# Optimization experiments

Hardware: AMD Instinct MI355X
Metric: run time of the kernel (lower is better)

The kernel has to match this reference:

```python
import jax, jax.numpy as jnp
import numpy as np

V = 6          # num_variables
K = 6          # codebook_size
D = 32         # embedding_dim
C = 3          # channels
B = 64         # batch
N = K ** V     # 46656 codebook combinations
EPS = 1e-5     # torch BatchNorm eps
ENTROPY_SCALE = 0.1


def setup_inputs() -> dict:
    key = jax.random.key(0)
    ks = jax.random.split(key, 40)
    i = iter(range(40))
    def rn(shape, s):
        return jax.random.normal(ks[next(i)], shape, dtype=jnp.float32) * s
    def rv(shape):
        return 0.5 + 0.5 * jax.random.uniform(ks[next(i)], shape, dtype=jnp.float32)
    inp = {
        'x': jax.random.normal(ks[next(i)], (B, C, 7, 7), dtype=jnp.float32),
        # encoder
        'conv_w': rn((256, C, 7, 7), 0.08), 'conv_b': rn((256,), 0.01),
        'ebn2_g': 1.0 + rn((256,), 0.1), 'ebn2_b': rn((256,), 0.1),
        'fc1_w': rn((1024, 256), 0.06), 'fc1_b': rn((1024,), 0.01),
        'ebn1_g': 1.0 + rn((1024,), 0.1), 'ebn1_b': rn((1024,), 0.1),
        'fc2_w': rn((V * K, 1024), 0.03), 'fc2_b': rn((V * K,), 0.01),
        # quantizer embeddings (V separate codebooks)
        'embeds': jax.random.normal(ks[next(i)], (V, K, D), dtype=jnp.float32),
        # decoder
        'dfc1_w': rn((1024, V * D), 0.07), 'dfc1_b': rn((1024,), 0.01),
        'dbn1_g': 1.0 + rn((1024,), 0.1), 'dbn1_b': rn((1024,), 0.1),
        'dbn1_rm': rn((1024,), 0.1), 'dbn1_rv': rv((1024,)),
        'dfc2_w': rn((256, 1024), 0.03), 'dfc2_b': rn((256,), 0.01),
        'dbn2_g': 1.0 + rn((256,), 0.1), 'dbn2_b': rn((256,), 0.1),
        'dbn2_rm': rn((256,), 0.1), 'dbn2_rv': rv((256,)),
        'dct1_w': rn((256, 16, 7, 7), 0.05), 'dct1_b': rn((16,), 0.01),
        'dbn3_g': 1.0 + rn((16,), 0.1), 'dbn3_b': rn((16,), 0.1),
        'dbn3_rm': rn((16,), 0.1), 'dbn3_rv': rv((16,)),
        'dct2_w': rn((16, C), 0.2), 'dct2_b': rn((C,), 0.01),
    }
    return inp


def _bn_eval(t, g, b, rm, rvar):
    # eval-mode BatchNorm (running stats); params broadcast over leading dims
    return g * (t - rm) * jax.lax.rsqrt(rvar + EPS) + b


def _bn_train(t, g, b):
    # train-mode BatchNorm1d on (B, F): biased batch statistics over dim 0
    m = t.mean(0)
    v = ((t - m) ** 2).mean(0)
    return g * (t - m) * jax.lax.rsqrt(v + EPS) + b


def _decode_all(embeds, dfc1_w, dfc1_b, dbn1_g, dbn1_b, dbn1_rm, dbn1_rv,
                dfc2_w, dfc2_b, dbn2_g, dbn2_b, dbn2_rm, dbn2_rv,
                dct1_w, dct1_b, dbn3_g, dbn3_b, dbn3_rm, dbn3_rv,
                dct2_w, dct2_b):
    # enumerate all K^V index tuples in itertools.product order (first var slowest)
    idx = jnp.arange(N)
    powers = K ** (V - 1 - jnp.arange(V))
    combos = (idx[:, None] // powers[None, :]) % K          # (N, V)
    z = embeds[jnp.arange(V)[None, :], combos]              # (N, V, D) gather
    h = z.reshape(N, V * D) @ dfc1_w.T + dfc1_b             # (N, 1024)
    h = jax.nn.relu(_bn_eval(h, dbn1_g, dbn1_b, dbn1_rm, dbn1_rv))
    h = h @ dfc2_w.T + dfc2_b                               # (N, 256)
    h = jax.nn.relu(_bn_eval(h, dbn2_g, dbn2_b, dbn2_rm, dbn2_rv))
    # ConvTranspose2d(256,16,7,stride=2) on 1x1 input == einsum with full kernel
    h = jnp.einsum('ni,iohw->nohw', h, dct1_w) + dct1_b[:, None, None]  # (N,16,7,7)
    h = jax.nn.relu(_bn_eval(h, dbn3_g[:, None, None], dbn3_b[:, None, None],
                             dbn3_rm[:, None, None], dbn3_rv[:, None, None]))
    # ConvTranspose2d(16,C,1,1) == pointwise channel mix
    em = jnp.einsum('nihw,io->nohw', h, dct2_w) + dct2_b[:, None, None]  # (N,C,7,7)
    return em


def reference(x, conv_w, conv_b, ebn2_g, ebn2_b, fc1_w, fc1_b, ebn1_g, ebn1_b,
              fc2_w, fc2_b, embeds, dfc1_w, dfc1_b, dbn1_g, dbn1_b, dbn1_rm,
              dbn1_rv, dfc2_w, dfc2_b, dbn2_g, dbn2_b, dbn2_rm, dbn2_rv,
              dct1_w, dct1_b, dbn3_g, dbn3_b, dbn3_rm, dbn3_rv, dct2_w, dct2_b):
    # emission means for every codebook combination (batched decode, BN eval)
    em = _decode_all(embeds, dfc1_w, dfc1_b, dbn1_g, dbn1_b, dbn1_rm, dbn1_rv,
                     dfc2_w, dfc2_b, dbn2_g, dbn2_b, dbn2_rm, dbn2_rv,
                     dct1_w, dct1_b, dbn3_g, dbn3_b, dbn3_rm, dbn3_rv,
                     dct2_w, dct2_b)                         # (N, C, 7, 7)
    # encoder: Conv2d(C,256,7) on 7x7 input collapses to a single GEMM
    e = jnp.einsum('bchw,ochw->bo', x, conv_w) + conv_b      # (B, 256)
    e = jax.nn.relu(_bn_train(e, ebn2_g, ebn2_b))
    e = e @ fc1_w.T + fc1_b                                  # (B, 1024)
    e = jax.nn.relu(_bn_train(e, ebn1_g, ebn1_b))
    logits = e @ fc2_w.T + fc2_b                             # (B, V*K)
    # quantizer
    latent_dist = jax.nn.softmax(logits.reshape(B, V, K), axis=-1)
    latent_loss = ENTROPY_SCALE * jnp.sum(
        latent_dist * jnp.log(latent_dist + 1e-10), axis=(1, 2))
    # obs logits: -0.5 * ||em - x||^2 summed over (C,H,W), via expanded form
    E = em.reshape(N, -1)                                    # (N, 147)
    X = x.reshape(B, -1)                                     # (B, 147)
    obs = -0.5 * (jnp.sum(E * E, -1)[None, :]
                  - 2.0 * (X @ E.T)
                  + jnp.sum(X * X, -1)[:, None])             # (B, N)
    obs_logits = obs.reshape((B,) + (K,) * V)
    return obs_logits, latent_dist, latent_loss
```

## Files before the change

kernel.cpp:

```cpp
#include <hip/hip_runtime.h>
#include <math.h>

#define EPSF 1e-5f
#define NNC 46656

typedef __attribute__((ext_vector_type(4))) float  f32x4;
typedef __attribute__((ext_vector_type(8))) short  short8;
typedef __attribute__((ext_vector_type(8))) unsigned short ushort8;
typedef __attribute__((ext_vector_type(4))) unsigned int uint4v;

__device__ __forceinline__ float bf2f(unsigned short u) {
    unsigned int x = ((unsigned int)u) << 16;
    return __builtin_bit_cast(float, x);
}
__device__ __forceinline__ unsigned short f2bf(float f) {
    unsigned int x = __builtin_bit_cast(unsigned int, f);
    unsigned int r = (x + 0x7fffu + ((x >> 16) & 1u)) >> 16;
    return (unsigned short)r;
}

__device__ __forceinline__ short8 packrelu8(ushort8 H8, ushort8 S8) {
    uint4v H = __builtin_bit_cast(uint4v, H8);
    uint4v S = __builtin_bit_cast(uint4v, S8);
    uint4v O;
#pragma unroll
    for (int d = 0; d < 4; ++d) {
        float hlo = __builtin_bit_cast(float, H[d] << 16);
        float hhi = __builtin_bit_cast(float, H[d] & 0xffff0000u);
        float slo = __builtin_bit_cast(float, S[d] << 16);
        float shi = __builtin_bit_cast(float, S[d] & 0xffff0000u);
        unsigned int rlo = __builtin_bit_cast(unsigned int, fmaxf(hlo + slo, 0.f));
        unsigned int rhi = __builtin_bit_cast(unsigned int, fmaxf(hhi + shi, 0.f));
        O[d] = __builtin_amdgcn_perm(rhi, rlo, 0x07060302u);
    }
    return __builtin_bit_cast(short8, O);
}

#define WS_SH    37888u
#define WS_S3    148480u
#define WS_W2BF  259072u
#define WS_C2    390144u
#define WS_W3BF  390400u
#define WS_C3    490752u
#define WS_XBF   490768u
#define WS_SX2   495888u
#define WS_E1T   495952u
#define WS_E2T   512336u
#define WS_FLAG  577872u

#define OBS_SIZE (64*NNC)
#define DIST_OFF OBS_SIZE
#define LOSS_OFF (OBS_SIZE + 64*36)

#define LDS_BYTES 75008


__global__ void dvae_k1(const float* __restrict__ x,
                        const float* __restrict__ conv_w, const float* __restrict__ conv_b,
                        const float* __restrict__ ebn2_g, const float* __restrict__ ebn2_b,
                        const float* __restrict__ embeds, const float* __restrict__ dfc1_w,
                        const float* __restrict__ dfc1_b,
                        const float* __restrict__ dbn1_g, const float* __restrict__ dbn1_b,
                        const float* __restrict__ dbn1_rm, const float* __restrict__ dbn1_rv,
                        const float* __restrict__ dfc2_w, const float* __restrict__ dfc2_b,
                        const float* __restrict__ dbn2_g, const float* __restrict__ dbn2_b,
                        const float* __restrict__ dbn2_rm, const float* __restrict__ dbn2_rv,
                        const float* __restrict__ dct1_w, const float* __restrict__ dct1_b,
                        const float* __restrict__ dbn3_g, const float* __restrict__ dbn3_b,
                        const float* __restrict__ dbn3_rm, const float* __restrict__ dbn3_rv,
                        float* __restrict__ ws) {
    __shared__ float sbuf[12544];
    int bx = blockIdx.x, tid = threadIdx.x;
    if (bx < 64) {
        float* wtile = sbuf;
        float* semb  = sbuf + 3088;
        float* Pt    = sbuf + 4240;
        float* c1s   = sbuf + 4960;
        int j0 = bx * 16;
        for (int e = tid; e < 16 * 192; e += 256)
            wtile[(e / 192) * 193 + (e % 192)] = dfc1_w[j0 * 192 + e];
        for (int e = tid; e < 1152; e += 256) semb[e] = embeds[e];
        __syncthreads();
        for (int e = tid; e < 576; e += 256) {
            int vk = e >> 4, jL = e & 15;
            int v = vk / 6;
            int j = j0 + jL;
            const float* wrow = &wtile[jL * 193 + v * 32];
            const float* ep = &semb[vk * 32];
            float dot = 0.f;
#pragma unroll
            for (int d = 0; d < 32; ++d) dot += wrow[d] * ep[d];
            float s1 = dbn1_g[j] * rsqrtf(dbn1_rv[j] + EPSF);
            Pt[vk * 20 + jL] = s1 * dot;
        }
        if (tid < 16) {
            int j = j0 + tid;
            float s = dbn1_g[j] * rsqrtf(dbn1_rv[j] + EPSF);
            c1s[tid] = s * dfc1_b[j] + dbn1_b[j] - dbn1_rm[j] * s;
        }
        __syncthreads();
        unsigned short* Sh = (unsigned short*)(ws + WS_SH);
        unsigned short* S3 = (unsigned short*)(ws + WS_S3);
        for (int e = tid; e < 216 * 16; e += 256) {
            int gh = e >> 4, jL = e & 15;
            int d0 = gh / 36, d1 = (gh / 6) % 6, d2 = gh % 6;
            float vh = c1s[jL] + Pt[d0 * 20 + jL] + Pt[(6 + d1) * 20 + jL] + Pt[(12 + d2) * 20 + jL];
            float vs = Pt[(18 + d0) * 20 + jL] + Pt[(24 + d1) * 20 + jL] + Pt[(30 + d2) * 20 + jL];
            Sh[gh * 1024 + j0 + jL] = f2bf(vh);
            S3[gh * 1024 + j0 + jL] = f2bf(vs);
        }
    } else if (bx < 320) {
        int t = (bx - 64) * 256 + tid;
        int i = t >> 8, kq = (t & 255) * 4;
        float s2 = dbn2_g[i] * rsqrtf(dbn2_rv[i] + EPSF);
        float4 w = *(const float4*)(dfc2_w + i * 1024 + kq);
        unsigned short* dst = (unsigned short*)(ws + WS_W2BF) + i * 1024 + kq;
        dst[0] = f2bf(s2 * w.x); dst[1] = f2bf(s2 * w.y);
        dst[2] = f2bf(s2 * w.z); dst[3] = f2bf(s2 * w.w);
        if (kq == 0) ws[WS_C2 + i] = s2 * dfc2_b[i] + dbn2_b[i] - dbn2_rm[i] * s2;
    } else if (bx < 336) {
        int blk = bx - 320;
        for (int e = tid; e < 12544; e += 256) sbuf[e] = dct1_w[blk * 12544 + e];
        __syncthreads();
        unsigned short* W3 = (unsigned short*)(ws + WS_W3BF);
        for (int e = tid; e < 1568; e += 256) {
            int up = e >> 1, k8 = (e & 1) * 8;
            int o = up & 15, hw = up >> 4;
            float s3 = dbn3_g[o] * rsqrtf(dbn3_rv[o] + EPSF);
            ushort8 ov;
#pragma unroll
            for (int t2 = 0; t2 < 8; ++t2)
                ov[t2] = f2bf(s3 * sbuf[(k8 + t2) * 784 + o * 49 + hw]);
            *(ushort8*)(W3 + up * 256 + blk * 16 + k8) = ov;
        }
        if (blk == 0 && tid < 16) {
            float s = dbn3_g[tid] * rsqrtf(dbn3_rv[tid] + EPSF);
            ws[WS_C3 + tid] = s * dct1_b[tid] + dbn3_b[tid] - dbn3_rm[tid] * s;
        }
    } else if (bx == 336) {
        unsigned short* Xb = (unsigned short*)(ws + WS_XBF);
        if (tid == 0) *(int*)(ws + WS_FLAG) = 0;
        if (tid < 64) {
            const float* xp = x + tid * 147;
            float s = 0.f;
            for (int qq = 0; qq < 147; ++qq) { float v = xp[qq]; s += v * v; }
            ws[WS_SX2 + tid] = s;
        }
        for (int e = tid; e < 64 * 160; e += 256) {
            int b = e / 160, col = e % 160;
            float v = 0.f;
            if (col < 147) { int hw = col / 3, c = col % 3; v = x[b * 147 + c * 49 + hw]; }
            Xb[e] = f2bf(v);
        }
    } else {
        int blk = bx - 337;
        for (int e = tid; e < 9408; e += 256) sbuf[e] = x[e];
        __syncthreads();
        int b = tid & 63;
        int oL = __builtin_amdgcn_readfirstlane(tid >> 6);
        int o = blk * 4 + oL;
        const float* wp = conv_w + o * 147;
        float acc = conv_b[o];
#pragma unroll 7
        for (int qq = 0; qq < 147; ++qq) acc += sbuf[b * 147 + qq] * wp[qq];
        float m = acc;
#pragma unroll
        for (int s = 1; s < 64; s <<= 1) m += __shfl_xor(m, s);
        m *= (1.f / 64.f);
        float d = acc - m;
        float var = d * d;
#pragma unroll
        for (int s = 1; s < 64; s <<= 1) var += __shfl_xor(var, s);
        var *= (1.f / 64.f);
        float y = ebn2_g[o] * d * rsqrtf(var + EPSF) + ebn2_b[o];
        ws[WS_E1T + o * 64 + b] = fmaxf(y, 0.f);
    }
}


__launch_bounds__(256, 2)
__global__ void dvae_k3(const unsigned short* __restrict__ Sh,
                        const unsigned short* __restrict__ S3g,
                        const unsigned short* __restrict__ W2,
                        const float* __restrict__ c2g,
                        const unsigned short* __restrict__ W3,
                        const float* __restrict__ c3g,
                        const float* __restrict__ d2wg,
                        const float* __restrict__ d2bg,
                        const unsigned short* __restrict__ Xg,
                        const float* __restrict__ sx2g,
                        const float* __restrict__ fc1_w, const float* __restrict__ fc1_b,
                        const float* __restrict__ ebn1_g, const float* __restrict__ ebn1_b,
                        const float* __restrict__ e1T,
                        float* __restrict__ e2T,
                        int* __restrict__ flag,
                        const float* __restrict__ fc2_w,
                        const float* __restrict__ fc2_b,
                        float* __restrict__ out) {
    extern __shared__ char sm[];
    int tid = threadIdx.x;

    if (blockIdx.x < 256) {
        int blk = blockIdx.x;
        int b = tid & 63;
        int jL = __builtin_amdgcn_readfirstlane(tid >> 6);
        int j = blk * 4 + jL;
        const float* wp = fc1_w + j * 256;
        float acc = fc1_b[j];
#pragma unroll 8
        for (int o = 0; o < 256; ++o) acc += e1T[o * 64 + b] * wp[o];
        float m = acc;
#pragma unroll
        for (int s = 1; s < 64; s <<= 1) m += __shfl_xor(m, s);
        m *= (1.f / 64.f);
        float d = acc - m;
        float var = d * d;
#pragma unroll
        for (int s = 1; s < 64; s <<= 1) var += __shfl_xor(var, s);
        var *= (1.f / 64.f);
        float y = ebn1_g[j] * d * rsqrtf(var + EPSF) + ebn1_b[j];
        e2T[j * 64 + b] = fmaxf(y, 0.f);
        __syncthreads();
        if (tid == 0) { __threadfence(); atomicAdd(flag, 1); }
        return;
    }

    if (blockIdx.x == 256) {
        if (tid == 0) {
            while (atomicAdd(flag, 0) < 256) __builtin_amdgcn_s_sleep(8);
        }
        __syncthreads();
        float* wch = (float*)sm;
        float* ech = (float*)(sm + 18432);
        float* LG  = (float*)(sm + 51200);
        int b = tid & 63;
        int wvU = __builtin_amdgcn_readfirstlane(tid >> 6);
        float accv[9];
#pragma unroll
        for (int it = 0; it < 9; ++it) accv[it] = 0.f;
        for (int ch = 0; ch < 8; ++ch) {
            __syncthreads();
            for (int e = tid; e < 36 * 128; e += 256)
                wch[e] = fc2_w[(e >> 7) * 1024 + ch * 128 + (e & 127)];
            for (int e = tid; e < 128 * 64; e += 256)
                ech[e] = e2T[(ch * 128 + (e >> 6)) * 64 + (e & 63)];
            __syncthreads();
            for (int jl = 0; jl < 128; ++jl) {
                float ev = ech[jl * 64 + b];
#pragma unroll
                for (int it = 0; it < 9; ++it)
                    accv[it] += ev * wch[(wvU + it * 4) * 128 + jl];
            }
        }
#pragma unroll
        for (int it = 0; it < 9; ++it) {
            int o = wvU + it * 4;
            LG[b * 36 + o] = accv[it] + fc2_b[o];
        }
        __syncthreads();
        if (tid < 64) {
            float loss = 0.f;
#pragma unroll
            for (int v = 0; v < 6; ++v) {
                float mx = -1e30f;
#pragma unroll
                for (int k = 0; k < 6; ++k) mx = fmaxf(mx, LG[tid * 36 + v * 6 + k]);
                float s = 0.f, ex[6];
#pragma unroll
                for (int k = 0; k < 6; ++k) { ex[k] = expf(LG[tid * 36 + v * 6 + k] - mx); s += ex[k]; }
                float inv = 1.f / s;
#pragma unroll
                for (int k = 0; k < 6; ++k) {
                    float dd = ex[k] * inv;
                    out[DIST_OFF + tid * 36 + v * 6 + k] = dd;
                    loss += dd * logf(dd + 1e-10f);
                }
            }
            out[LOSS_OFF + tid] = 0.1f * loss;
        }
        return;
    }

    int wv = tid >> 6, lane = tid & 63, l15 = lane & 15, q = lane >> 4;
    int nbase = (blockIdx.x - 257) * 64;
    float* sE2p = (float*)(sm + 0);
    float* sE2f = (float*)(sm + 1024);
    unsigned short* emL = (unsigned short*)(sm + 1280);
    float* h3w = (float*)(sm + 21760 + wv * 5120);
    unsigned short* h2L = (unsigned short*)(sm + 42240);

    f32x4 acc[4][4];
#pragma unroll
    for (int a = 0; a < 4; ++a)
#pragma unroll
        for (int b = 0; b < 4; ++b) acc[a][b] = (f32x4){0.f, 0.f, 0.f, 0.f};

    const unsigned short* pSh[4];
    const unsigned short* pS3[4];
#pragma unroll
    for (int mt = 0; mt < 4; ++mt) {
        int nm = nbase + mt * 16 + l15;
        int gh = nm / 216;
        int r216 = nm - gh * 216;
        pSh[mt] = Sh + gh * 1024 + q * 8;
        pS3[mt] = S3g + r216 * 1024 + q * 8;
    }
    const unsigned short* bbase = W2 + (wv * 64 + l15) * 1024 + q * 8;

    ushort8 sa[4], sb[4];
    short8 bpre[4];
#pragma unroll
    for (int mt = 0; mt < 4; ++mt) { sa[mt] = *(const ushort8*)(pSh[mt]); sb[mt] = *(const ushort8*)(pS3[mt]); }
#pragma unroll
    for (int j = 0; j < 4; ++j) bpre[j] = *(const short8*)(bbase + j * 16384);

#pragma unroll 2
    for (int s = 0; s < 32; ++s) {
        short8 af[4];
#pragma unroll
        for (int mt = 0; mt < 4; ++mt) af[mt] = packrelu8(sa[mt], sb[mt]);
        short8 bcur[4];
#pragma unroll
        for (int j = 0; j < 4; ++j) bcur[j] = bpre[j];
        if (s < 31) {
            int off = (s + 1) * 32;
#pragma unroll
            for (int mt = 0; mt < 4; ++mt) {
                sa[mt] = *(const ushort8*)(pSh[mt] + off);
                sb[mt] = *(const ushort8*)(pS3[mt] + off);
            }
#pragma unroll
            for (int j = 0; j < 4; ++j) bpre[j] = *(const short8*)(bbase + j * 16384 + off);
        }
#pragma unroll
        for (int mt = 0; mt < 4; ++mt)
#pragma unroll
            for (int j = 0; j < 4; ++j)
                acc[mt][j] = __builtin_amdgcn_mfma_f32_16x16x32_bf16(af[mt], bcur[j], acc[mt][j], 0, 0, 0);
    }
#pragma unroll
    for (int j = 0; j < 4; ++j) {
        int i = wv * 64 + j * 16 + l15;
        float cc = c2g[i];
#pragma unroll
        for (int mt = 0; mt < 4; ++mt)
#pragma unroll
            for (int r = 0; r < 4; ++r) {
                int m = mt * 16 + q * 4 + r;
                h2L[((i >> 3) * 64 + m) * 8 + (i & 7)] = f2bf(fmaxf(acc[mt][j][r] + cc, 0.f));
            }
    }
    __syncthreads();

    float c3v = c3g[l15];
    float db0 = d2bg[0], db1 = d2bg[1], db2 = d2bg[2];
    float dw0[16], dw1[16], dw2[16];
#pragma unroll
    for (int o = 0; o < 16; ++o) {
        dw0[o] = d2wg[o * 3 + 0]; dw1[o] = d2wg[o * 3 + 1]; dw2[o] = d2wg[o * 3 + 2];
    }
    float sE2a = 0.f;
    for (int c = wv; c < 13; c += 4) {
        int hw0 = c * 4;
        f32x4 a2[4][4];
#pragma unroll
        for (int a = 0; a < 4; ++a)
#pragma unroll
            for (int b = 0; b < 4; ++b) a2[a][b] = (f32x4){0.f, 0.f, 0.f, 0.f};
        const unsigned short* b3[4];
#pragma unroll
        for (int j = 0; j < 4; ++j) {
            int hw = hw0 + j; if (hw > 48) hw = 48;
            b3[j] = W3 + (hw * 16 + l15) * 256 + q * 8;
        }
        short8 bpre2[4];
#pragma unroll
        for (int j = 0; j < 4; ++j) bpre2[j] = *(const short8*)(b3[j]);
#pragma unroll
        for (int s = 0; s < 8; ++s) {
            short8 bcur[4];
#pragma unroll
            for (int j = 0; j < 4; ++j) bcur[j] = bpre2[j];
            if (s < 7) {
#pragma unroll
                for (int j = 0; j < 4; ++j) bpre2[j] = *(const short8*)(b3[j] + (s + 1) * 32);
            }
            short8 af[4];
#pragma unroll
            for (int mt = 0; mt < 4; ++mt)
                af[mt] = *(const short8*)(h2L + ((s * 4 + q) * 64 + mt * 16 + l15) * 8);
#pragma unroll
            for (int mt = 0; mt < 4; ++mt)
#pragma unroll
                for (int j = 0; j < 4; ++j)
                    a2[mt][j] = __builtin_amdgcn_mfma_f32_16x16x32_bf16(af[mt], bcur[j], a2[mt][j], 0, 0, 0);
        }
#pragma unroll
        for (int j = 0; j < 4; ++j) {
            int hw = hw0 + j;
            if (hw <= 48) {
#pragma unroll
                for (int mt = 0; mt < 4; ++mt)
#pragma unroll
                    for (int r = 0; r < 4; ++r)
                        h3w[(mt * 16 + q * 4 + r) * 20 + l15] = fmaxf(a2[mt][j][r] + c3v, 0.f);
                float hvv[16];
#pragma unroll
                for (int g = 0; g < 4; ++g) {
                    f32x4 tv = *(const f32x4*)(h3w + lane * 20 + g * 4);
                    hvv[g * 4 + 0] = tv[0]; hvv[g * 4 + 1] = tv[1];
                    hvv[g * 4 + 2] = tv[2]; hvv[g * 4 + 3] = tv[3];
                }
                float e0 = db0, e1 = db1, e2 = db2;
#pragma unroll
                for (int o = 0; o < 16; ++o) {
                    e0 += hvv[o] * dw0[o]; e1 += hvv[o] * dw1[o]; e2 += hvv[o] * dw2[o];
                }
                unsigned short u0 = f2bf(e0), u1 = f2bf(e1), u2 = f2bf(e2);
                float f0 = bf2f(u0), f1 = bf2f(u1), f2v = bf2f(u2);
                sE2a += f0 * f0 + f1 * f1 + f2v * f2v;
                emL[lane * 160 + hw * 3 + 0] = u0;
                emL[lane * 160 + hw * 3 + 1] = u1;
                emL[lane * 160 + hw * 3 + 2] = u2;
            }
        }
    }
    sE2p[wv * 64 + lane] = sE2a;
    for (int e = tid; e < 64 * 13; e += 256) emL[(e / 13) * 160 + 147 + (e % 13)] = 0;
    __syncthreads();
    if (tid < 64) sE2f[tid] = sE2p[tid] + sE2p[64 + tid] + sE2p[128 + tid] + sE2p[192 + tid];
    __syncthreads();

    f32x4 aO[4];
#pragma unroll
    for (int j = 0; j < 4; ++j) aO[j] = (f32x4){0.f, 0.f, 0.f, 0.f};
    const unsigned short* xrow = Xg + (wv * 16 + l15) * 160 + q * 8;
#pragma unroll
    for (int s = 0; s < 5; ++s) {
        short8 af = *(const short8*)(xrow + s * 32);
#pragma unroll
        for (int j = 0; j < 4; ++j) {
            short8 bfv = *(const short8*)(emL + (j * 16 + l15) * 160 + s * 32 + q * 8);
            aO[j] = __builtin_amdgcn_mfma_f32_16x16x32_bf16(af, bfv, aO[j], 0, 0, 0);
        }
    }
    int b0 = wv * 16 + q * 4;
    float sxv[4];
#pragma unroll
    for (int r = 0; r < 4; ++r) sxv[r] = sx2g[b0 + r];
#pragma unroll
    for (int j = 0; j < 4; ++j) {
        int n = nbase + j * 16 + l15;
        float he = 0.5f * sE2f[j * 16 + l15];
#pragma unroll
        for (int r = 0; r < 4; ++r)
            out[(size_t)(b0 + r) * NNC + n] = aO[j][r] - he - 0.5f * sxv[r];
    }
}


extern "C" void kernel_launch(void* const* d_in, const int* in_sizes, int n_in,
                              void* d_out, int out_size, void* d_ws, size_t ws_size,
                              hipStream_t stream) {
    const float* x       = (const float*)d_in[0];
    const float* conv_w  = (const float*)d_in[1];
    const float* conv_b  = (const float*)d_in[2];
    const float* ebn2_g  = (const float*)d_in[3];
    const float* ebn2_b  = (const float*)d_in[4];
    const float* fc1_w   = (const float*)d_in[5];
    const float* fc1_b   = (const float*)d_in[6];
    const float* ebn1_g  = (const float*)d_in[7];
    const float* ebn1_b  = (const float*)d_in[8];
    const float* fc2_w   = (const float*)d_in[9];
    const float* fc2_b   = (const float*)d_in[10];
    const float* embeds  = (const float*)d_in[11];
    const float* dfc1_w  = (const float*)d_in[12];
    const float* dfc1_b  = (const float*)d_in[13];
    const float* dbn1_g  = (const float*)d_in[14];
    const float* dbn1_b  = (const float*)d_in[15];
    const float* dbn1_rm = (const float*)d_in[16];
    const float* dbn1_rv = (const float*)d_in[17];
    const float* dfc2_w  = (const float*)d_in[18];
    const float* dfc2_b  = (const float*)d_in[19];
    const float* dbn2_g  = (const float*)d_in[20];
    const float* dbn2_b  = (const float*)d_in[21];
    const float* dbn2_rm = (const float*)d_in[22];
    const float* dbn2_rv = (const float*)d_in[23];
    const float* dct1_w  = (const float*)d_in[24];
    const float* dct1_b  = (const float*)d_in[25];
    const float* dbn3_g  = (const float*)d_in[26];
    const float* dbn3_b  = (const float*)d_in[27];
    const float* dbn3_rm = (const float*)d_in[28];
    const float* dbn3_rv = (const float*)d_in[29];
    const float* dct2_w  = (const float*)d_in[30];
    const float* dct2_b  = (const float*)d_in[31];

    float* ws  = (float*)d_ws;
    float* out = (float*)d_out;

    dvae_k1<<<401, 256, 0, stream>>>(x, conv_w, conv_b, ebn2_g, ebn2_b,
                                     embeds, dfc1_w, dfc1_b, dbn1_g, dbn1_b, dbn1_rm, dbn1_rv,
                                     dfc2_w, dfc2_b, dbn2_g, dbn2_b, dbn2_rm, dbn2_rv,
                                     dct1_w, dct1_b, dbn3_g, dbn3_b, dbn3_rm, dbn3_rv, ws);

    hipFuncSetAttribute(reinterpret_cast<const void*>(dvae_k3),
                        hipFuncAttributeMaxDynamicSharedMemorySize, LDS_BYTES);
    dvae_k3<<<986, 256, LDS_BYTES, stream>>>(
        (const unsigned short*)(ws + WS_SH), (const unsigned short*)(ws + WS_S3),
        (const unsigned short*)(ws + WS_W2BF), ws + WS_C2,
        (const unsigned short*)(ws + WS_W3BF), ws + WS_C3,
        dct2_w, dct2_b,
        (const unsigned short*)(ws + WS_XBF), ws + WS_SX2,
        fc1_w, fc1_b, ebn1_g, ebn1_b,
        ws + WS_E1T, ws + WS_E2T, (int*)(ws + WS_FLAG),
        fc2_w, fc2_b, out);
}
```

Before: 273.1 us.

## Tile decoder rows as 8x8 factor blocks and stage relu-packed A in LDS

```diff
diff --git a/kernel.cpp b/kernel.cpp
--- a/kernel.cpp
+++ b/kernel.cpp
@@ -282,12 +282,14 @@
     }
 
     int wv = tid >> 6, lane = tid & 63, l15 = lane & 15, q = lane >> 4;
-    int nbase = (blockIdx.x - 257) * 64;
+    int db = blockIdx.x - 257;
+    int g0 = (db / 27) * 8, r0 = (db % 27) * 8;
     float* sE2p = (float*)(sm + 0);
     float* sE2f = (float*)(sm + 1024);
     unsigned short* emL = (unsigned short*)(sm + 1280);
     float* h3w = (float*)(sm + 21760 + wv * 5120);
     unsigned short* h2L = (unsigned short*)(sm + 42240);
+    char* Ast = sm + 1280;
 
     f32x4 acc[4][4];
 #pragma unroll
@@ -295,49 +297,68 @@
 #pragma unroll
         for (int b = 0; b < 4; ++b) acc[a][b] = (f32x4){0.f, 0.f, 0.f, 0.f};
 
-    const unsigned short* pSh[4];
-    const unsigned short* pS3[4];
-#pragma unroll
-    for (int mt = 0; mt < 4; ++mt) {
-        int nm = nbase + mt * 16 + l15;
-        int gh = nm / 216;
-        int r216 = nm - gh * 216;
-        pSh[mt] = Sh + gh * 1024 + q * 8;
-        pS3[mt] = S3g + r216 * 1024 + q * 8;
-    }
+    int gh_t = g0 + (lane >> 3);
+    int r_t  = r0 + (lane & 7);
+    const unsigned short* shp = Sh  + gh_t * 1024 + wv * 32;
+    const unsigned short* s3p = S3g + r_t  * 1024 + wv * 32;
     const unsigned short* bbase = W2 + (wv * 64 + l15) * 1024 + q * 8;
-
-    ushort8 sa[4], sb[4];
+    int Xw = (lane & 7) << 4;
+    int Xr = (l15 & 7) << 4;
+
+    ushort8 rsh[4], rs3[4];
+#pragma unroll
+    for (int i = 0; i < 4; ++i) {
+        rsh[i] = *(const ushort8*)(shp + i * 8);
+        rs3[i] = *(const ushort8*)(s3p + i * 8);
+    }
     short8 bpre[4];
 #pragma unroll
-    for (int mt = 0; mt < 4; ++mt) { sa[mt] = *(const ushort8*)(pSh[mt]); sb[mt] = *(const ushort8*)(pS3[mt]); }
-#pragma unroll
     for (int j = 0; j < 4; ++j) bpre[j] = *(const short8*)(bbase + j * 16384);
-
-#pragma unroll 2
-    for (int s = 0; s < 32; ++s) {
-        short8 af[4];
-#pragma unroll
-        for (int mt = 0; mt < 4; ++mt) af[mt] = packrelu8(sa[mt], sb[mt]);
-        short8 bcur[4];
-#pragma unroll
-        for (int j = 0; j < 4; ++j) bcur[j] = bpre[j];
-        if (s < 31) {
-            int off = (s + 1) * 32;
-#pragma unroll
-            for (int mt = 0; mt < 4; ++mt) {
-                sa[mt] = *(const ushort8*)(pSh[mt] + off);
-                sb[mt] = *(const ushort8*)(pS3[mt] + off);
-            }
-#pragma unroll
-            for (int j = 0; j < 4; ++j) bpre[j] = *(const short8*)(bbase + j * 16384 + off);
-        }
-#pragma unroll
-        for (int mt = 0; mt < 4; ++mt)
-#pragma unroll
-            for (int j = 0; j < 4; ++j)
-                acc[mt][j] = __builtin_amdgcn_mfma_f32_16x16x32_bf16(af[mt], bcur[j], acc[mt][j], 0, 0, 0);
-    }
+#pragma unroll
+    for (int i = 0; i < 4; ++i)
+        *(short8*)(Ast + lane * 256 + ((wv * 64 + i * 16) ^ Xw)) = packrelu8(rsh[i], rs3[i]);
+    __syncthreads();
+
+    for (int c = 0; c < 8; ++c) {
+        int cb = (c & 1) << 14;
+        if (c < 7) {
+            const unsigned short* p1 = shp + (c + 1) * 128;
+            const unsigned short* p3 = s3p + (c + 1) * 128;
+#pragma unroll
+            for (int i = 0; i < 4; ++i) {
+                rsh[i] = *(const ushort8*)(p1 + i * 8);
+                rs3[i] = *(const ushort8*)(p3 + i * 8);
+            }
+        }
+#pragma unroll
+        for (int ss = 0; ss < 4; ++ss) {
+            int s = c * 4 + ss;
+            short8 af[4];
+#pragma unroll
+            for (int mt = 0; mt < 4; ++mt)
+                af[mt] = *(const short8*)(Ast + cb + (mt * 16 + l15) * 256 + ((ss * 64 + q * 16) ^ Xr));
+            short8 bcur[4];
+#pragma unroll
+            for (int j = 0; j < 4; ++j) bcur[j] = bpre[j];
+            if (s < 31) {
+#pragma unroll
+                for (int j = 0; j < 4; ++j) bpre[j] = *(const short8*)(bbase + j * 16384 + (s + 1) * 32);
+            }
+#pragma unroll
+            for (int mt = 0; mt < 4; ++mt)
+#pragma unroll
+                for (int j = 0; j < 4; ++j)
+                    acc[mt][j] = __builtin_amdgcn_mfma_f32_16x16x32_bf16(af[mt], bcur[j], acc[mt][j], 0, 0, 0);
+        }
+        if (c < 7) {
+            int nb = ((c + 1) & 1) << 14;
+#pragma unroll
+            for (int i = 0; i < 4; ++i)
+                *(short8*)(Ast + nb + lane * 256 + ((wv * 64 + i * 16) ^ Xw)) = packrelu8(rsh[i], rs3[i]);
+        }
+        __syncthreads();
+    }
+
 #pragma unroll
     for (int j = 0; j < 4; ++j) {
         int i = wv * 64 + j * 16 + l15;
@@ -450,8 +471,9 @@
     for (int r = 0; r < 4; ++r) sxv[r] = sx2g[b0 + r];
 #pragma unroll
     for (int j = 0; j < 4; ++j) {
-        int n = nbase + j * 16 + l15;
-        float he = 0.5f * sE2f[j * 16 + l15];
+        int rloc = j * 16 + l15;
+        int n = (g0 + (rloc >> 3)) * 216 + r0 + (rloc & 7);
+        float he = 0.5f * sE2f[rloc];
 #pragma unroll
         for (int r = 0; r < 4; ++r)
             out[(size_t)(b0 + r) * NNC + n] = aO[j][r] - he - 0.5f * sxv[r];
```

Result: faster. 260.6 us (-4.6%).
